# Kernel optimization log

Measured on AMD Instinct MI355X. Metric: run time of the kernel, lower is better.

The kernel has to match this reference:

```python
import jax, jax.numpy as jnp
import numpy as np

H = 128          # hidden_size == in_channels == graph_hidden_size
P = 16           # pair_neurons
B = 4096         # number of graph pairs
T = 262144       # total nodes per side
V_D, V_P, V_A = 10000, 4000, 4000          # leaf vocab sizes
NG_D, NG_P, NG_A = 13000, 5200, 5200       # DAG graph node counts
L_D, L_P, L_A = 4, 4, 5                    # ancestor levels
TOTAL_V = V_D + V_P + V_A                  # 18000 rows in all_embedding


def setup_inputs() -> dict:
    key = jax.random.key(0)
    ks = jax.random.split(key, 40)
    n = lambda i, shape, s: jax.random.normal(ks[i], shape, jnp.float32) * s
    ri = lambda i, shape, hi: jax.random.randint(ks[i], shape, 0, hi, dtype=jnp.int64)
    inp = {}
    # forward args
    inp["left_x"] = ri(0, (T, 1), TOTAL_V)
    inp["left_graph_index"] = ri(1, (B,), B)
    inp["right_x"] = ri(2, (T, 1), TOTAL_V)
    inp["right_graph_index"] = ri(3, (B,), B)
    inp["left_x_batch"] = jnp.sort(ri(4, (T,), B))
    inp["right_x_batch"] = jnp.sort(ri(5, (T,), B))
    inp["left_diag_cnt"] = ri(6, (B,), 64)
    inp["right_diag_cnt"] = ri(7, (B,), 64)
    # DAG structure buffers (built by build_ancestors in the original)
    inp["anc_d"] = ri(8, (V_D, L_D), NG_D)
    inp["leaf_d"] = ri(9, (V_D, L_D), NG_D)
    inp["anc_p"] = ri(10, (V_P, L_P), NG_P)
    inp["leaf_p"] = ri(11, (V_P, L_P), NG_P)
    inp["anc_a"] = ri(12, (V_A, L_A), NG_A)
    inp["leaf_a"] = ri(13, (V_A, L_A), NG_A)
    # learned parameters
    inp["emb_d"] = n(14, (NG_D, H), 0.1)
    inp["emb_p"] = n(15, (NG_P, H), 0.1)
    inp["emb_a"] = n(16, (NG_A, H), 0.1)
    inp["Wl_d"] = n(17, (H, 2 * H), 0.05); inp["bl_d"] = n(18, (H,), 0.05); inp["ap_d"] = n(19, (H, 1), 0.05)
    inp["Wl_p"] = n(20, (H, 2 * H), 0.05); inp["bl_p"] = n(21, (H,), 0.05); inp["ap_p"] = n(22, (H, 1), 0.05)
    inp["Wl_a"] = n(23, (H, 2 * H), 0.05); inp["bl_a"] = n(24, (H,), 0.05); inp["ap_a"] = n(25, (H, 1), 0.05)
    inp["W_ntn"] = n(26, (H, H, P), 0.02)
    inp["V_ntn"] = n(27, (P, 2 * H), 0.02)
    inp["b_ntn"] = n(28, (P,), 0.02)
    inp["w_fc"] = n(29, (1, P), 0.1)
    inp["b_fc"] = n(30, (1,), 0.1)
    return inp


def _dag_embedding(emb, anc, leaf, Wl, bl, ap):
    # emb: [Ng,H]; anc/leaf: [V,L] int
    anc_e = emb[anc]    # [V,L,H]
    leaf_e = emb[leaf]  # [V,L,H]
    h = jnp.tanh(jnp.concatenate([anc_e, leaf_e], axis=-1) @ Wl.T + bl)  # [V,L,H]
    aw = (h @ ap)[..., 0]                     # [V,L]
    s = jax.nn.softmax(aw, axis=-1)           # [V,L]
    # torch.matmul((V,L),(V,L,C)).sum(dim=1) == einsum('l,vlc->vc', s.sum(0), anc_e)
    return jnp.einsum('l,vlc->vc', s.sum(axis=0), anc_e)  # [V,H]


def reference(left_x, left_graph_index, right_x, right_graph_index,
              left_x_batch, right_x_batch, left_diag_cnt, right_diag_cnt,
              anc_d, leaf_d, anc_p, leaf_p, anc_a, leaf_a,
              emb_d, emb_p, emb_a,
              Wl_d, bl_d, ap_d, Wl_p, bl_p, ap_p, Wl_a, bl_a, ap_a,
              W_ntn, V_ntn, b_ntn, w_fc, b_fc):
    all_emb = jnp.concatenate([
        _dag_embedding(emb_d, anc_d, leaf_d, Wl_d, bl_d, ap_d),
        _dag_embedding(emb_p, anc_p, leaf_p, Wl_p, bl_p, ap_p),
        _dag_embedding(emb_a, anc_a, leaf_a, Wl_a, bl_a, ap_a),
    ], axis=0)                                  # [TOTAL_V, H]
    left_onto = all_emb[left_x[:, 0]]           # [T,H]
    right_onto = all_emb[right_x[:, 0]]         # [T,H]
    le = jax.ops.segment_sum(left_onto, left_x_batch, num_segments=B)    # [B,H]
    re = jax.ops.segment_sum(right_onto, right_x_batch, num_segments=B)  # [B,H]
    # Neural tensor similarity: tanh(e1^T W_k e2 + V [e1;e2] + b)
    bilinear = jnp.einsum('bi,ijp,bj->bp', le, W_ntn, re)                # [B,P]
    block = jnp.concatenate([le, re], axis=-1) @ V_ntn.T                 # [B,P]
    pair_sim = jnp.tanh(bilinear + block + b_ntn)                        # [B,P]
    out = jax.nn.sigmoid(pair_sim @ w_fc.T + b_fc)[:, 0]                 # [B]
    return out
```

## Files before the change

### kernel.cpp

```cpp
#include <hip/hip_runtime.h>
#include <hip/hip_bf16.h>

typedef __hip_bfloat16 bf16;
typedef __attribute__((ext_vector_type(8))) short bf16x8;
typedef __attribute__((ext_vector_type(4))) float f32x4;

#define HID 128
#define PD  16
#define BB  4096
#define TT  262144
#define VD  10000
#define VP  4000
#define VA  4000
#define NGD 13000
#define NGP 5200
#define NGA 5200

#define NB_D ((NGD + 31) / 32)
#define NB_P ((NGP + 31) / 32)
#define NB_A ((NGA + 31) / 32)

__device__ __forceinline__ float2 bf2x(unsigned int u) {
    float lo = __uint_as_float(u << 16);
    float hi = __uint_as_float(u & 0xffff0000u);
    return make_float2(lo, hi);
}

union Pack2 { bf16 h[2]; unsigned int u; };
__device__ __forceinline__ unsigned int pk2(float a, float b) {
    Pack2 p; p.h[0] = __float2bfloat16(a); p.h[1] = __float2bfloat16(b); return p.u;
}

__global__ __launch_bounds__(256) void prep_b3(
    const float* __restrict__ Wl_d, const float* __restrict__ Wl_p, const float* __restrict__ Wl_a,
    bf16* __restrict__ B3_d, bf16* __restrict__ B3_p, bf16* __restrict__ B3_a)
{
    const int sec = blockIdx.x >> 4, jt = blockIdx.x & 15;
    const float* Wl = (sec == 0) ? Wl_d : (sec == 1) ? Wl_p : Wl_a;
    bf16* B3 = (sec == 0) ? B3_d : (sec == 1) ? B3_p : B3_a;
    const int tid = threadIdx.x;
    const int q = tid >> 6, lane = tid & 63;
    const int quad = lane >> 4, m = lane & 15;
    const int col = jt * 16 + m;
    const float* src = (col < 128) ? (Wl + col * 256) : (Wl + (col - 128) * 256 + 128);
    unsigned int pk[4];
#pragma unroll
    for (int jp = 0; jp < 4; ++jp) {
        int k0 = q * 32 + quad * 8 + 2 * jp;
        pk[jp] = pk2(src[k0], src[k0 + 1]);
    }
    uint4 val = make_uint4(pk[0], pk[1], pk[2], pk[3]);
    *reinterpret_cast<uint4*>(B3 + ((size_t)(jt * 4 + q) * 64 + lane) * 8) = val;
}

__device__ __forceinline__ void stage1_body(
    unsigned short (*Abf)[136],
    const float* __restrict__ emb, const bf16* __restrict__ B3,
    bf16* __restrict__ U, int NG, int blk)
{
    const int tid  = threadIdx.x;
    const int row0 = blk * 32;
    {
        const int r = tid >> 3, seg = tid & 7;
        const int g = row0 + r;
        float v[16];
        if (g < NG) {
            const float4* src = reinterpret_cast<const float4*>(emb + (size_t)g * HID + seg * 16);
#pragma unroll
            for (int i = 0; i < 4; ++i) {
                float4 f = src[i];
                v[4 * i] = f.x; v[4 * i + 1] = f.y; v[4 * i + 2] = f.z; v[4 * i + 3] = f.w;
            }
        } else {
#pragma unroll
            for (int i = 0; i < 16; ++i) v[i] = 0.f;
        }
        unsigned int pk[8];
#pragma unroll
        for (int i = 0; i < 8; ++i) pk[i] = pk2(v[2 * i], v[2 * i + 1]);
        uint4* dst = reinterpret_cast<uint4*>(&Abf[r][seg * 16]);
        dst[0] = make_uint4(pk[0], pk[1], pk[2], pk[3]);
        dst[1] = make_uint4(pk[4], pk[5], pk[6], pk[7]);
    }
    __syncthreads();

    const int lane   = tid & 63;
    const int w      = tid >> 6;
    const int gtile  = w & 1;
    const int jstrip = w >> 1;
    const int lrow   = gtile * 16 + (lane & 15);
    const int koff   = (lane >> 4) * 8;
    const bf16x8* B3f = reinterpret_cast<const bf16x8*>(B3);

    f32x4 acc[8];
#pragma unroll
    for (int t = 0; t < 8; ++t) acc[t] = (f32x4){0.f, 0.f, 0.f, 0.f};

#pragma unroll
    for (int q = 0; q < 4; ++q) {
        bf16x8 ef = *reinterpret_cast<const bf16x8*>(&Abf[lrow][q * 32 + koff]);
#pragma unroll
        for (int t = 0; t < 8; ++t) {
            int jt = jstrip * 8 + t;
            bf16x8 wf = B3f[(jt * 4 + q) * 64 + lane];
            acc[t] = __builtin_amdgcn_mfma_f32_16x16x32_bf16(wf, ef, acc[t], 0, 0, 0);
        }
    }

    const int g = row0 + gtile * 16 + (lane & 15);
    if (g < NG) {
        const int quad = lane >> 4;
        bf16* Ur = U + (size_t)g * 256;
#pragma unroll
        for (int t = 0; t < 8; ++t) {
            int j0 = (jstrip * 8 + t) * 16 + quad * 4;
            uint2 st = make_uint2(pk2(acc[t].x, acc[t].y), pk2(acc[t].z, acc[t].w));
            *reinterpret_cast<uint2*>(Ur + j0) = st;
        }
    }
}

__global__ __launch_bounds__(256) void stage1_mfma(
    const float* __restrict__ emb_d, const bf16* __restrict__ B3_d, bf16* __restrict__ U_d,
    const float* __restrict__ emb_p, const bf16* __restrict__ B3_p, bf16* __restrict__ U_p,
    const float* __restrict__ emb_a, const bf16* __restrict__ B3_a, bf16* __restrict__ U_a)
{
    __shared__ unsigned short Abf[32][136];
    int bx = blockIdx.x;
    if (bx < NB_D)             stage1_body(Abf, emb_d, B3_d, U_d, NGD, bx);
    else if (bx < NB_D + NB_P) stage1_body(Abf, emb_p, B3_p, U_p, NGP, bx - NB_D);
    else                       stage1_body(Abf, emb_a, B3_a, U_a, NGA, bx - NB_D - NB_P);
}

template <int L>
__device__ __forceinline__ void aw_body(
    float* sacc,
    const bf16* __restrict__ U, const int* __restrict__ anc, const int* __restrict__ leaf,
    const float* __restrict__ bl, const float* __restrict__ ap,
    float* __restrict__ s_out, int V, int blk, int nblk)
{
    const int tid  = threadIdx.x;
    const int lane = tid & 63;
    const int wid  = blk * 4 + (tid >> 6);
    const int nw   = nblk * 4;
    const float2 blv = *reinterpret_cast<const float2*>(bl + 2 * lane);
    const float2 apv = *reinterpret_cast<const float2*>(ap + 2 * lane);
    const unsigned int* Uw = reinterpret_cast<const unsigned int*>(U);
    float wacc[L];
#pragma unroll
    for (int l = 0; l < L; ++l) wacc[l] = 0.f;

    for (int vp = wid; vp < V / 2; vp += nw) {
        const int v0 = 2 * vp;
        int a0[L], f0[L], a1[L], f1[L];
        if (L == 4) {
            int4 ia = *reinterpret_cast<const int4*>(anc  + (size_t)v0 * 4);
            int4 ib = *reinterpret_cast<const int4*>(anc  + (size_t)v0 * 4 + 4);
            int4 fa = *reinterpret_cast<const int4*>(leaf + (size_t)v0 * 4);
            int4 fb = *reinterpret_cast<const int4*>(leaf + (size_t)v0 * 4 + 4);
            a0[0] = ia.x; a0[1] = ia.y; a0[2] = ia.z; a0[3] = ia.w;
            a1[0] = ib.x; a1[1] = ib.y; a1[2] = ib.z; a1[3] = ib.w;
            f0[0] = fa.x; f0[1] = fa.y; f0[2] = fa.z; f0[3] = fa.w;
            f1[0] = fb.x; f1[1] = fb.y; f1[2] = fb.z; f1[3] = fb.w;
        } else {
#pragma unroll
            for (int l = 0; l < L; ++l) {
                a0[l] = anc[(size_t)v0 * L + l];
                a1[l] = anc[(size_t)(v0 + 1) * L + l];
                f0[l] = leaf[(size_t)v0 * L + l];
                f1[l] = leaf[(size_t)(v0 + 1) * L + l];
            }
        }
        unsigned int ua0[L], ul0[L], ua1[L], ul1[L];
#pragma unroll
        for (int l = 0; l < L; ++l) {
            ua0[l] = Uw[(size_t)a0[l] * 128 + lane];
            ul0[l] = Uw[(size_t)f0[l] * 128 + 64 + lane];
            ua1[l] = Uw[(size_t)a1[l] * 128 + lane];
            ul1[l] = Uw[(size_t)f1[l] * 128 + 64 + lane];
        }
        float aw0[L], aw1[L];
#pragma unroll
        for (int l = 0; l < L; ++l) {
            float2 x0 = bf2x(ua0[l]), y0 = bf2x(ul0[l]);
            float2 x1 = bf2x(ua1[l]), y1 = bf2x(ul1[l]);
            float p0 = tanhf(x0.x + y0.x + blv.x) * apv.x + tanhf(x0.y + y0.y + blv.y) * apv.y;
            float p1 = tanhf(x1.x + y1.x + blv.x) * apv.x + tanhf(x1.y + y1.y + blv.y) * apv.y;
#pragma unroll
            for (int off = 32; off; off >>= 1) {
                p0 += __shfl_xor(p0, off, 64);
                p1 += __shfl_xor(p1, off, 64);
            }
            aw0[l] = p0; aw1[l] = p1;
        }
        float m0 = aw0[0], m1 = aw1[0];
#pragma unroll
        for (int l = 1; l < L; ++l) { m0 = fmaxf(m0, aw0[l]); m1 = fmaxf(m1, aw1[l]); }
        float d0 = 0.f, d1 = 0.f, e0[L], e1[L];
#pragma unroll
        for (int l = 0; l < L; ++l) {
            e0[l] = __expf(aw0[l] - m0); d0 += e0[l];
            e1[l] = __expf(aw1[l] - m1); d1 += e1[l];
        }
        float i0 = 1.f / d0, i1 = 1.f / d1;
#pragma unroll
        for (int l = 0; l < L; ++l) wacc[l] += e0[l] * i0 + e1[l] * i1;
    }
    if (lane == 0) {
#pragma unroll
        for (int l = 0; l < L; ++l) atomicAdd(&sacc[l], wacc[l]);
    }
    __syncthreads();
    if (tid < L) atomicAdd(&s_out[tid], sacc[tid]);
}

__global__ __launch_bounds__(256) void aw_all(
    const bf16* __restrict__ U_d, const int* __restrict__ anc_d, const int* __restrict__ leaf_d,
    const float* __restrict__ bl_d, const float* __restrict__ ap_d,
    const bf16* __restrict__ U_p, const int* __restrict__ anc_p, const int* __restrict__ leaf_p,
    const float* __restrict__ bl_p, const float* __restrict__ ap_p,
    const bf16* __restrict__ U_a, const int* __restrict__ anc_a, const int* __restrict__ leaf_a,
    const float* __restrict__ bl_a, const float* __restrict__ ap_a,
    float* __restrict__ s_sum)
{
    __shared__ float sacc[5];
    const int tid = threadIdx.x;
    if (tid < 5) sacc[tid] = 0.f;
    __syncthreads();
    int bx = blockIdx.x;
    if (bx < 512)      aw_body<4>(sacc, U_d, anc_d, leaf_d, bl_d, ap_d, s_sum + 0, VD, bx, 512);
    else if (bx < 768) aw_body<4>(sacc, U_p, anc_p, leaf_p, bl_p, ap_p, s_sum + 4, VP, bx - 512, 256);
    else               aw_body<5>(sacc, U_a, anc_a, leaf_a, bl_a, ap_a, s_sum + 8, VA, bx - 768, 256);
}

template <int L>
__device__ __forceinline__ void allemb_body(
    const float* __restrict__ emb, const int* __restrict__ anc,
    const float* __restrict__ s, float* __restrict__ out, int V, int blk, int nblk)
{
    const int tid   = threadIdx.x;
    const int lane4 = tid & 31;
    const int vslot = tid >> 5;
    const float4* emb4 = reinterpret_cast<const float4*>(emb);
    float4* out4 = reinterpret_cast<float4*>(out);
    float sv[L];
#pragma unroll
    for (int l = 0; l < L; ++l) sv[l] = s[l];
    for (int vp = blk * 8 + vslot; vp < V / 2; vp += nblk * 8) {
        const int v0 = 2 * vp;
        int a0[L], a1[L];
        if (L == 4) {
            int4 ia = *reinterpret_cast<const int4*>(anc + (size_t)v0 * 4);
            int4 ib = *reinterpret_cast<const int4*>(anc + (size_t)v0 * 4 + 4);
            a0[0] = ia.x; a0[1] = ia.y; a0[2] = ia.z; a0[3] = ia.w;
            a1[0] = ib.x; a1[1] = ib.y; a1[2] = ib.z; a1[3] = ib.w;
        } else {
#pragma unroll
            for (int l = 0; l < L; ++l) {
                a0[l] = anc[(size_t)v0 * L + l];
                a1[l] = anc[(size_t)(v0 + 1) * L + l];
            }
        }
        float4 e0[L], e1[L];
#pragma unroll
        for (int l = 0; l < L; ++l) {
            e0[l] = emb4[(size_t)a0[l] * 32 + lane4];
            e1[l] = emb4[(size_t)a1[l] * 32 + lane4];
        }
        float4 r0 = make_float4(0.f, 0.f, 0.f, 0.f);
        float4 r1 = make_float4(0.f, 0.f, 0.f, 0.f);
#pragma unroll
        for (int l = 0; l < L; ++l) {
            r0.x += sv[l] * e0[l].x; r0.y += sv[l] * e0[l].y;
            r0.z += sv[l] * e0[l].z; r0.w += sv[l] * e0[l].w;
            r1.x += sv[l] * e1[l].x; r1.y += sv[l] * e1[l].y;
            r1.z += sv[l] * e1[l].z; r1.w += sv[l] * e1[l].w;
        }
        out4[(size_t)v0 * 32 + lane4]       = r0;
        out4[(size_t)(v0 + 1) * 32 + lane4] = r1;
    }
}

__global__ __launch_bounds__(256) void allemb_all(
    const float* __restrict__ emb_d, const int* __restrict__ anc_d,
    const float* __restrict__ emb_p, const int* __restrict__ anc_p,
    const float* __restrict__ emb_a, const int* __restrict__ anc_a,
    const float* __restrict__ s_sum, float* __restrict__ all_emb)
{
    int bx = blockIdx.x;
    if (bx < 512)
        allemb_body<4>(emb_d, anc_d, s_sum + 0, all_emb, VD, bx, 512);
    else if (bx < 768)
        allemb_body<4>(emb_p, anc_p, s_sum + 4, all_emb + (size_t)VD * HID, VP, bx - 512, 256);
    else
        allemb_body<5>(emb_a, anc_a, s_sum + 8, all_emb + (size_t)(VD + VP) * HID, VA, bx - 768, 256);
}

__global__ __launch_bounds__(256) void seg_bounds(
    const int* __restrict__ lb, const int* __restrict__ rb,
    int* __restrict__ segL, int* __restrict__ segR, float* __restrict__ s_sum)
{
    int gid = blockIdx.x * 256 + threadIdx.x;
    if (gid >= 2 * BB + 8 && gid < 2 * BB + 24) s_sum[gid - (2 * BB + 8)] = 0.f;
    const int* batch;
    int* segp;
    int b;
    if (gid <= BB) { batch = lb; segp = segL; b = gid; }
    else if (gid <= 2 * BB + 1) { batch = rb; segp = segR; b = gid - BB - 1; }
    else return;
    int l = 0, r = TT;
    while (l < r) { int m = (l + r) >> 1; if (batch[m] < b) l = m + 1; else r = m; }
    segp[b] = l;
}

__global__ __launch_bounds__(256) void segsum_mlp(
    const float* __restrict__ all_emb,
    const int* __restrict__ lx, const int* __restrict__ segL, float* __restrict__ le,
    const int* __restrict__ rx, const int* __restrict__ segR, float* __restrict__ re)
{
    __shared__ float4 red[4][32];
    const int tid  = threadIdx.x;
    const int b    = blockIdx.x & (BB - 1);
    const int lane = tid & 63;
    const int w    = tid >> 6;
    const int* x;
    const int* seg;
    float* out;
    if (blockIdx.x < BB) { x = lx; seg = segL; out = le; }
    else                 { x = rx; seg = segR; out = re; }
    const int lo = seg[b], hi = seg[b + 1];
    const int half  = lane >> 5;
    const int lane4 = lane & 31;
    const float4* AE4 = reinterpret_cast<const float4*>(all_emb);
    float4 acc = make_float4(0.f, 0.f, 0.f, 0.f);

    for (int tb = lo + 16 * w; tb < hi; tb += 64) {
        int idxv = x[min(tb + (lane & 15), hi - 1)];
        float4 v[8];
        int val[8];
#pragma unroll
        for (int u = 0; u < 8; ++u) {
            int src = 2 * u + half;
            int ridx = __shfl(idxv, src, 64);
            val[u] = (tb + src) < hi;
            v[u] = AE4[(size_t)ridx * 32 + lane4];
        }
#pragma unroll
        for (int u = 0; u < 8; ++u) {
            if (val[u]) {
                acc.x += v[u].x; acc.y += v[u].y;
                acc.z += v[u].z; acc.w += v[u].w;
            }
        }
    }
    acc.x += __shfl_xor(acc.x, 32, 64);
    acc.y += __shfl_xor(acc.y, 32, 64);
    acc.z += __shfl_xor(acc.z, 32, 64);
    acc.w += __shfl_xor(acc.w, 32, 64);
    if (lane < 32) red[w][lane4] = acc;
    __syncthreads();
    if (tid < 32) {
        float4 r0 = red[0][tid], r1 = red[1][tid], r2 = red[2][tid], r3 = red[3][tid];
        float4 s;
        s.x = r0.x + r1.x + r2.x + r3.x;
        s.y = r0.y + r1.y + r2.y + r3.y;
        s.z = r0.z + r1.z + r2.z + r3.z;
        s.w = r0.w + r1.w + r2.w + r3.w;
        reinterpret_cast<float4*>(out)[(size_t)b * 32 + tid] = s;
    }
}

__global__ __launch_bounds__(256) void ntn_part(
    const float* __restrict__ le, const float* __restrict__ re,
    const float* __restrict__ W2, float* __restrict__ part)
{
    __shared__ float Alds[64][33];
    __shared__ float Blds[32 * 256];
    __shared__ float Rlds[64][17];
    const int tid   = threadIdx.x;
    const int row0  = blockIdx.x * 64;
    const int ch    = blockIdx.y;
    const int col0  = ch * 256;
    const int lane5 = tid & 31;
    const int h     = tid >> 5;
    const int rbase = h * 8;
    float acc[8][8];
#pragma unroll
    for (int i = 0; i < 8; ++i)
#pragma unroll
        for (int j = 0; j < 8; ++j) acc[i][j] = 0.f;

    for (int i = tid; i < 64 * 16; i += 256) {
        int rr = i >> 4, jl = i & 15;
        Rlds[rr][jl] = re[(size_t)(row0 + rr) * HID + ch * 16 + jl];
    }

    for (int k0 = 0; k0 < 128; k0 += 32) {
        __syncthreads();
        {
            const int rr = tid >> 5, kk = tid & 31;
#pragma unroll
            for (int it = 0; it < 8; ++it)
                Alds[rr + it * 8][kk] = le[(size_t)(row0 + rr + it * 8) * HID + k0 + kk];
        }
        for (int i = tid; i < 32 * 64; i += 256) {
            int kk = i >> 6, j4 = (i & 63) * 4;
            float4 v = *reinterpret_cast<const float4*>(&W2[(size_t)(k0 + kk) * 2048 + col0 + j4]);
            *reinterpret_cast<float4*>(&Blds[kk * 256 + j4]) = v;
        }
        __syncthreads();
#pragma unroll
        for (int kk = 0; kk < 32; ++kk) {
            float4 blo = *reinterpret_cast<const float4*>(&Blds[kk * 256 + 4 * lane5]);
            float4 bhi = *reinterpret_cast<const float4*>(&Blds[kk * 256 + 128 + 4 * lane5]);
            float bv[8] = {blo.x, blo.y, blo.z, blo.w, bhi.x, bhi.y, bhi.z, bhi.w};
#pragma unroll
            for (int i = 0; i < 8; ++i) {
                float a = Alds[rbase + i][kk];
#pragma unroll
                for (int j = 0; j < 8; ++j) acc[i][j] += a * bv[j];
            }
        }
    }

    const int q = lane5 >> 2;
#pragma unroll
    for (int r = 0; r < 8; ++r) {
        float rlo = Rlds[rbase + r][q];
        float rhi = Rlds[rbase + r][8 + q];
        float pb[4];
#pragma unroll
        for (int d = 0; d < 4; ++d) pb[d] = acc[r][d] * rlo + acc[r][4 + d] * rhi;
#pragma unroll
        for (int m = 4; m <= 16; m <<= 1) {
#pragma unroll
            for (int d = 0; d < 4; ++d) pb[d] += __shfl_xor(pb[d], m, 64);
        }
        if (lane5 < 4) {
            size_t base = ((size_t)ch * BB + row0 + rbase + r) * PD + 4 * lane5;
            *reinterpret_cast<float4*>(&part[base]) = make_float4(pb[0], pb[1], pb[2], pb[3]);
        }
    }
}

__global__ __launch_bounds__(256) void ntn_epi(
    const float* __restrict__ part, const float* __restrict__ le, const float* __restrict__ re,
    const float* __restrict__ Vntn, const float* __restrict__ bntn,
    const float* __restrict__ wfc, const float* __restrict__ bfc,
    float* __restrict__ out)
{
    __shared__ float Vlds[16 * 257];
    __shared__ float LE[16 * 128];
    __shared__ float RE[16 * 128];
    const int tid = threadIdx.x;
    const int b0  = blockIdx.x * 16;
    for (int i = tid; i < 4096; i += 256) Vlds[(i >> 8) * 257 + (i & 255)] = Vntn[i];
    for (int i = tid; i < 2048; i += 256) {
        LE[i] = le[(size_t)b0 * HID + i];
        RE[i] = re[(size_t)b0 * HID + i];
    }
    __syncthreads();
    const int bl = tid >> 4, p = tid & 15;
    const int b  = b0 + bl;
    float bil = 0.f;
#pragma unroll
    for (int by = 0; by < 8; ++by) bil += part[((size_t)by * BB + b) * PD + p];
    float s = bil + bntn[p];
    const float* Vp   = &Vlds[p * 257];
    const float* lrow = &LE[bl * 128];
    const float* rrow = &RE[bl * 128];
#pragma unroll 8
    for (int c = 0; c < 128; ++c) s += lrow[c] * Vp[c] + rrow[c] * Vp[128 + c];
    float x = tanhf(s) * wfc[p];
    x += __shfl_xor(x, 1, 64);
    x += __shfl_xor(x, 2, 64);
    x += __shfl_xor(x, 4, 64);
    x += __shfl_xor(x, 8, 64);
    if (p == 0) out[b] = 1.f / (1.f + __expf(-(x + bfc[0])));
}

extern "C" void kernel_launch(void* const* d_in, const int* in_sizes, int n_in,
                              void* d_out, int out_size, void* d_ws, size_t ws_size,
                              hipStream_t stream)
{
    const int* left_x      = (const int*)d_in[0];
    const int* right_x     = (const int*)d_in[2];
    const int* left_batch  = (const int*)d_in[4];
    const int* right_batch = (const int*)d_in[5];
    const int* anc_d  = (const int*)d_in[8];
    const int* leaf_d = (const int*)d_in[9];
    const int* anc_p  = (const int*)d_in[10];
    const int* leaf_p = (const int*)d_in[11];
    const int* anc_a  = (const int*)d_in[12];
    const int* leaf_a = (const int*)d_in[13];
    const float* emb_d = (const float*)d_in[14];
    const float* emb_p = (const float*)d_in[15];
    const float* emb_a = (const float*)d_in[16];
    const float* Wl_d = (const float*)d_in[17];
    const float* bl_d = (const float*)d_in[18];
    const float* ap_d = (const float*)d_in[19];
    const float* Wl_p = (const float*)d_in[20];
    const float* bl_p = (const float*)d_in[21];
    const float* ap_p = (const float*)d_in[22];
    const float* Wl_a = (const float*)d_in[23];
    const float* bl_a = (const float*)d_in[24];
    const float* ap_a = (const float*)d_in[25];
    const float* W_ntn = (const float*)d_in[26];
    const float* V_ntn = (const float*)d_in[27];
    const float* b_ntn = (const float*)d_in[28];
    const float* w_fc  = (const float*)d_in[29];
    const float* b_fc  = (const float*)d_in[30];
    float* out = (float*)d_out;

    float* ws = (float*)d_ws;
    float* s_sum   = ws;
    float* le      = ws + 64;
    float* re      = le + (size_t)BB * HID;
    float* all_emb = re + (size_t)BB * HID;
    float* part    = all_emb + (size_t)(VD + VP + VA) * HID;
    int*   segL    = (int*)(part + (size_t)8 * BB * PD);
    int*   segR    = segL + 4100;
    bf16*  U       = (bf16*)(segR + 4100);
    bf16*  U_d = U;
    bf16*  U_p = U_d + (size_t)NGD * 256;
    bf16*  U_a = U_p + (size_t)NGP * 256;
    bf16*  B3_d = U_a + (size_t)NGA * 256;
    bf16*  B3_p = B3_d + 32768;
    bf16*  B3_a = B3_p + 32768;

    prep_b3<<<48, 256, 0, stream>>>(Wl_d, Wl_p, Wl_a, B3_d, B3_p, B3_a);

    seg_bounds<<<33, 256, 0, stream>>>(left_batch, right_batch, segL, segR, s_sum);

    stage1_mfma<<<NB_D + NB_P + NB_A, 256, 0, stream>>>(
        emb_d, B3_d, U_d, emb_p, B3_p, U_p, emb_a, B3_a, U_a);

    aw_all<<<1024, 256, 0, stream>>>(
        U_d, anc_d, leaf_d, bl_d, ap_d,
        U_p, anc_p, leaf_p, bl_p, ap_p,
        U_a, anc_a, leaf_a, bl_a, ap_a, s_sum);

    allemb_all<<<1024, 256, 0, stream>>>(
        emb_d, anc_d, emb_p, anc_p, emb_a, anc_a, s_sum, all_emb);

    segsum_mlp<<<2 * BB, 256, 0, stream>>>(
        all_emb, left_x, segL, le, right_x, segR, re);

    ntn_part<<<dim3(64, 8), 256, 0, stream>>>(le, re, W_ntn, part);

    ntn_epi<<<BB / 16, 256, 0, stream>>>(part, le, re, V_ntn, b_ntn, w_fc, b_fc, out);
}
```

Measured before the change: 236.5 us.

## Run NTN bilinear on bf16x3 MFMA and merge prologue kernels

Replaces the FP32 scalar-FMA bilinear GEMM in the NTN stage with MFMA bf16 instructions. It splits both the W_ntn weights and the left embeddings into three bf16 parts (high, mid, low) and sums six cross-product MFMAs so accuracy stays close to fp32. The weight split and fragment packing happen in a new prologue kernel, which also absorbs the B3 prep and segment-bounds kernels, so there are fewer launches. The cost is six MFMAs per tile instead of one, plus extra workspace for the three split weight copies.

```diff
diff --git a/kernel.cpp b/kernel.cpp
--- a/kernel.cpp
+++ b/kernel.cpp
@@ -30,27 +30,77 @@
 __device__ __forceinline__ unsigned int pk2(float a, float b) {
     Pack2 p; p.h[0] = __float2bfloat16(a); p.h[1] = __float2bfloat16(b); return p.u;
 }
-
-__global__ __launch_bounds__(256) void prep_b3(
+__device__ __forceinline__ short bfs(float x) {
+    bf16 h = __float2bfloat16(x);
+    return *reinterpret_cast<short*>(&h);
+}
+union FragU { short s[8]; bf16x8 v; uint4 u; };
+
+__global__ __launch_bounds__(256) void prologue(
     const float* __restrict__ Wl_d, const float* __restrict__ Wl_p, const float* __restrict__ Wl_a,
-    bf16* __restrict__ B3_d, bf16* __restrict__ B3_p, bf16* __restrict__ B3_a)
-{
-    const int sec = blockIdx.x >> 4, jt = blockIdx.x & 15;
-    const float* Wl = (sec == 0) ? Wl_d : (sec == 1) ? Wl_p : Wl_a;
-    bf16* B3 = (sec == 0) ? B3_d : (sec == 1) ? B3_p : B3_a;
+    bf16* __restrict__ B3_d, bf16* __restrict__ B3_p, bf16* __restrict__ B3_a,
+    const int* __restrict__ lb, const int* __restrict__ rb,
+    int* __restrict__ segL, int* __restrict__ segR, float* __restrict__ s_sum,
+    const float* __restrict__ W2,
+    bf16* __restrict__ W3h, bf16* __restrict__ W3m, bf16* __restrict__ W3l)
+{
+    __shared__ float LW[128][17];
+    const int bx = blockIdx.x;
     const int tid = threadIdx.x;
-    const int q = tid >> 6, lane = tid & 63;
-    const int quad = lane >> 4, m = lane & 15;
-    const int col = jt * 16 + m;
-    const float* src = (col < 128) ? (Wl + col * 256) : (Wl + (col - 128) * 256 + 128);
-    unsigned int pk[4];
-#pragma unroll
-    for (int jp = 0; jp < 4; ++jp) {
-        int k0 = q * 32 + quad * 8 + 2 * jp;
-        pk[jp] = pk2(src[k0], src[k0 + 1]);
-    }
-    uint4 val = make_uint4(pk[0], pk[1], pk[2], pk[3]);
-    *reinterpret_cast<uint4*>(B3 + ((size_t)(jt * 4 + q) * 64 + lane) * 8) = val;
+    if (bx < 48) {
+        const int sec = bx >> 4, jt = bx & 15;
+        const float* Wl = (sec == 0) ? Wl_d : (sec == 1) ? Wl_p : Wl_a;
+        bf16* B3 = (sec == 0) ? B3_d : (sec == 1) ? B3_p : B3_a;
+        const int q = tid >> 6, lane = tid & 63;
+        const int quad = lane >> 4, m = lane & 15;
+        const int col = jt * 16 + m;
+        const float* src = (col < 128) ? (Wl + col * 256) : (Wl + (col - 128) * 256 + 128);
+        unsigned int pk[4];
+#pragma unroll
+        for (int jp = 0; jp < 4; ++jp) {
+            int k0 = q * 32 + quad * 8 + 2 * jp;
+            pk[jp] = pk2(src[k0], src[k0 + 1]);
+        }
+        uint4 val = make_uint4(pk[0], pk[1], pk[2], pk[3]);
+        *reinterpret_cast<uint4*>(B3 + ((size_t)(jt * 4 + q) * 64 + lane) * 8) = val;
+    } else if (bx < 81) {
+        int gid = (bx - 48) * 256 + tid;
+        if (gid >= 2 * BB + 8 && gid < 2 * BB + 24) s_sum[gid - (2 * BB + 8)] = 0.f;
+        const int* batch;
+        int* segp;
+        int b;
+        if (gid <= BB) { batch = lb; segp = segL; b = gid; }
+        else if (gid <= 2 * BB + 1) { batch = rb; segp = segR; b = gid - BB - 1; }
+        else return;
+        int l = 0, r = TT;
+        while (l < r) { int m2 = (l + r) >> 1; if (batch[m2] < b) l = m2 + 1; else r = m2; }
+        segp[b] = l;
+    } else {
+        const int t = bx - 81;
+        for (int idx = tid; idx < 2048; idx += 256) {
+            int k = idx >> 4, m = idx & 15;
+            LW[k][m] = W2[(size_t)k * 2048 + 16 * t + m];
+        }
+        __syncthreads();
+        const int q = tid >> 6, lane = tid & 63;
+        const int m = lane & 15, quad = lane >> 4;
+        FragU fh, fm, fl;
+#pragma unroll
+        for (int j = 0; j < 8; ++j) {
+            float x = LW[32 * q + quad * 8 + j][m];
+            bf16 h = __float2bfloat16(x);
+            float r = x - __bfloat162float(h);
+            bf16 md = __float2bfloat16(r);
+            float r2 = r - __bfloat162float(md);
+            fh.s[j] = *reinterpret_cast<short*>(&h);
+            fm.s[j] = *reinterpret_cast<short*>(&md);
+            fl.s[j] = bfs(r2);
+        }
+        size_t off = ((size_t)(t * 4 + q) * 64 + lane) * 8;
+        *reinterpret_cast<uint4*>(W3h + off) = fh.u;
+        *reinterpret_cast<uint4*>(W3m + off) = fm.u;
+        *reinterpret_cast<uint4*>(W3l + off) = fl.u;
+    }
 }
 
 __device__ __forceinline__ void stage1_body(
@@ -294,23 +344,6 @@
         allemb_body<4>(emb_p, anc_p, s_sum + 4, all_emb + (size_t)VD * HID, VP, bx - 512, 256);
     else
         allemb_body<5>(emb_a, anc_a, s_sum + 8, all_emb + (size_t)(VD + VP) * HID, VA, bx - 768, 256);
-}
-
-__global__ __launch_bounds__(256) void seg_bounds(
-    const int* __restrict__ lb, const int* __restrict__ rb,
-    int* __restrict__ segL, int* __restrict__ segR, float* __restrict__ s_sum)
-{
-    int gid = blockIdx.x * 256 + threadIdx.x;
-    if (gid >= 2 * BB + 8 && gid < 2 * BB + 24) s_sum[gid - (2 * BB + 8)] = 0.f;
-    const int* batch;
-    int* segp;
-    int b;
-    if (gid <= BB) { batch = lb; segp = segL; b = gid; }
-    else if (gid <= 2 * BB + 1) { batch = rb; segp = segR; b = gid - BB - 1; }
-    else return;
-    int l = 0, r = TT;
-    while (l < r) { int m = (l + r) >> 1; if (batch[m] < b) l = m + 1; else r = m; }
-    segp[b] = l;
 }
 
 __global__ __launch_bounds__(256) void segsum_mlp(
@@ -370,77 +403,79 @@
     }
 }
 
-__global__ __launch_bounds__(256) void ntn_part(
+__global__ __launch_bounds__(256) void ntn_mfma(
     const float* __restrict__ le, const float* __restrict__ re,
-    const float* __restrict__ W2, float* __restrict__ part)
-{
-    __shared__ float Alds[64][33];
-    __shared__ float Blds[32 * 256];
+    const bf16* __restrict__ W3h, const bf16* __restrict__ W3m, const bf16* __restrict__ W3l,
+    float* __restrict__ part)
+{
     __shared__ float Rlds[64][17];
-    const int tid   = threadIdx.x;
-    const int row0  = blockIdx.x * 64;
-    const int ch    = blockIdx.y;
-    const int col0  = ch * 256;
-    const int lane5 = tid & 31;
-    const int h     = tid >> 5;
-    const int rbase = h * 8;
-    float acc[8][8];
-#pragma unroll
-    for (int i = 0; i < 8; ++i)
-#pragma unroll
-        for (int j = 0; j < 8; ++j) acc[i][j] = 0.f;
-
-    for (int i = tid; i < 64 * 16; i += 256) {
-        int rr = i >> 4, jl = i & 15;
-        Rlds[rr][jl] = re[(size_t)(row0 + rr) * HID + ch * 16 + jl];
-    }
-
-    for (int k0 = 0; k0 < 128; k0 += 32) {
-        __syncthreads();
-        {
-            const int rr = tid >> 5, kk = tid & 31;
-#pragma unroll
-            for (int it = 0; it < 8; ++it)
-                Alds[rr + it * 8][kk] = le[(size_t)(row0 + rr + it * 8) * HID + k0 + kk];
-        }
-        for (int i = tid; i < 32 * 64; i += 256) {
-            int kk = i >> 6, j4 = (i & 63) * 4;
-            float4 v = *reinterpret_cast<const float4*>(&W2[(size_t)(k0 + kk) * 2048 + col0 + j4]);
-            *reinterpret_cast<float4*>(&Blds[kk * 256 + j4]) = v;
-        }
-        __syncthreads();
-#pragma unroll
-        for (int kk = 0; kk < 32; ++kk) {
-            float4 blo = *reinterpret_cast<const float4*>(&Blds[kk * 256 + 4 * lane5]);
-            float4 bhi = *reinterpret_cast<const float4*>(&Blds[kk * 256 + 128 + 4 * lane5]);
-            float bv[8] = {blo.x, blo.y, blo.z, blo.w, bhi.x, bhi.y, bhi.z, bhi.w};
-#pragma unroll
-            for (int i = 0; i < 8; ++i) {
-                float a = Alds[rbase + i][kk];
-#pragma unroll
-                for (int j = 0; j < 8; ++j) acc[i][j] += a * bv[j];
+    const int tid  = threadIdx.x;
+    const int bg   = blockIdx.x;
+    const int ch   = blockIdx.y;
+    const int w    = tid >> 6;
+    const int lane = tid & 63;
+    const int m    = lane & 15;
+    const int quad = lane >> 4;
+    const int rb   = bg * 64 + w * 16 + m;
+
+    for (int idx = tid; idx < 1024; idx += 256) {
+        int row = idx >> 4, jl = idx & 15;
+        Rlds[row][jl] = re[(size_t)(bg * 64 + row) * HID + ch * 16 + jl];
+    }
+
+    bf16x8 lh[4], lm[4], ll[4];
+    {
+        const float* lp = le + (size_t)rb * HID + quad * 8;
+#pragma unroll
+        for (int q = 0; q < 4; ++q) {
+            float4 f0 = *reinterpret_cast<const float4*>(lp + 32 * q);
+            float4 f1 = *reinterpret_cast<const float4*>(lp + 32 * q + 4);
+            float x[8] = {f0.x, f0.y, f0.z, f0.w, f1.x, f1.y, f1.z, f1.w};
+            FragU fh, fm, fl;
+#pragma unroll
+            for (int j = 0; j < 8; ++j) {
+                bf16 h = __float2bfloat16(x[j]);
+                float r = x[j] - __bfloat162float(h);
+                bf16 md = __float2bfloat16(r);
+                float r2 = r - __bfloat162float(md);
+                fh.s[j] = *reinterpret_cast<short*>(&h);
+                fm.s[j] = *reinterpret_cast<short*>(&md);
+                fl.s[j] = bfs(r2);
             }
-        }
-    }
-
-    const int q = lane5 >> 2;
-#pragma unroll
-    for (int r = 0; r < 8; ++r) {
-        float rlo = Rlds[rbase + r][q];
-        float rhi = Rlds[rbase + r][8 + q];
-        float pb[4];
-#pragma unroll
-        for (int d = 0; d < 4; ++d) pb[d] = acc[r][d] * rlo + acc[r][4 + d] * rhi;
-#pragma unroll
-        for (int m = 4; m <= 16; m <<= 1) {
-#pragma unroll
-            for (int d = 0; d < 4; ++d) pb[d] += __shfl_xor(pb[d], m, 64);
-        }
-        if (lane5 < 4) {
-            size_t base = ((size_t)ch * BB + row0 + rbase + r) * PD + 4 * lane5;
-            *reinterpret_cast<float4*>(&part[base]) = make_float4(pb[0], pb[1], pb[2], pb[3]);
-        }
-    }
+            lh[q] = fh.v; lm[q] = fm.v; ll[q] = fl.v;
+        }
+    }
+    __syncthreads();
+
+    const bf16x8* Whf = reinterpret_cast<const bf16x8*>(W3h);
+    const bf16x8* Wmf = reinterpret_cast<const bf16x8*>(W3m);
+    const bf16x8* Wlf = reinterpret_cast<const bf16x8*>(W3l);
+
+    float blin[4] = {0.f, 0.f, 0.f, 0.f};
+#pragma unroll 2
+    for (int tl = 0; tl < 16; ++tl) {
+        const int t = ch * 16 + tl;
+        f32x4 acc = (f32x4){0.f, 0.f, 0.f, 0.f};
+#pragma unroll
+        for (int q = 0; q < 4; ++q) {
+            const int fi = (t * 4 + q) * 64 + lane;
+            bf16x8 wh = Whf[fi], wm = Wmf[fi], wl = Wlf[fi];
+            acc = __builtin_amdgcn_mfma_f32_16x16x32_bf16(wh, lh[q], acc, 0, 0, 0);
+            acc = __builtin_amdgcn_mfma_f32_16x16x32_bf16(wh, lm[q], acc, 0, 0, 0);
+            acc = __builtin_amdgcn_mfma_f32_16x16x32_bf16(wm, lh[q], acc, 0, 0, 0);
+            acc = __builtin_amdgcn_mfma_f32_16x16x32_bf16(wh, ll[q], acc, 0, 0, 0);
+            acc = __builtin_amdgcn_mfma_f32_16x16x32_bf16(wl, lh[q], acc, 0, 0, 0);
+            acc = __builtin_amdgcn_mfma_f32_16x16x32_bf16(wm, lm[q], acc, 0, 0, 0);
+        }
+        float rt = Rlds[w * 16 + m][tl];
+        blin[0] += acc.x * rt;
+        blin[1] += acc.y * rt;
+        blin[2] += acc.z * rt;
+        blin[3] += acc.w * rt;
+    }
+
+    size_t base = ((size_t)ch * BB + rb) * PD + quad * 4;
+    *reinterpret_cast<float4*>(&part[base]) = make_float4(blin[0], blin[1], blin[2], blin[3]);
 }
 
 __global__ __launch_bounds__(256) void ntn_epi(
@@ -527,10 +562,14 @@
     bf16*  B3_d = U_a + (size_t)NGA * 256;
     bf16*  B3_p = B3_d + 32768;
     bf16*  B3_a = B3_p + 32768;
-
-    prep_b3<<<48, 256, 0, stream>>>(Wl_d, Wl_p, Wl_a, B3_d, B3_p, B3_a);
-
-    seg_bounds<<<33, 256, 0, stream>>>(left_batch, right_batch, segL, segR, s_sum);
+    bf16*  W3h  = B3_a + 32768;
+    bf16*  W3m  = W3h + 262144;
+    bf16*  W3l  = W3m + 262144;
+
+    prologue<<<209, 256, 0, stream>>>(
+        Wl_d, Wl_p, Wl_a, B3_d, B3_p, B3_a,
+        left_batch, right_batch, segL, segR, s_sum,
+        W_ntn, W3h, W3m, W3l);
 
     stage1_mfma<<<NB_D + NB_P + NB_A, 256, 0, stream>>>(
         emb_d, B3_d, U_d, emb_p, B3_p, U_p, emb_a, B3_a, U_a);
@@ -546,7 +585,7 @@
     segsum_mlp<<<2 * BB, 256, 0, stream>>>(
         all_emb, left_x, segL, le, right_x, segR, re);
 
-    ntn_part<<<dim3(64, 8), 256, 0, stream>>>(le, re, W_ntn, part);
+    ntn_mfma<<<dim3(64, 8), 256, 0, stream>>>(le, re, W3h, W3m, W3l, part);
 
     ntn_epi<<<BB / 16, 256, 0, stream>>>(part, le, re, V_ntn, b_ntn, w_fc, b_fc, out);
 }
```

New measurement: 223.5 us, median of 2. -5.5%, faster.
